# Performance work log

Hardware: AMD Instinct MI355X
Metric: run time of the kernel (lower is better)

## Reference

```python
import jax, jax.numpy as jnp
import numpy as np

N_EMBD = 1024
N_HEAD = 16
HEAD_SIZE = N_EMBD // N_HEAD
B, T = 2, 2048
LN_EPS = 1e-5


def _layernorm(x, g, b):
    mu = jnp.mean(x, axis=-1, keepdims=True)
    var = jnp.var(x, axis=-1, keepdims=True)
    return (x - mu) * jax.lax.rsqrt(var + LN_EPS) * g + b


def setup_inputs() -> dict:
    key = jax.random.key(0)
    ks = jax.random.split(key, 12)
    s_in = 1.0 / np.sqrt(N_EMBD)
    s_ff = 1.0 / np.sqrt(4 * N_EMBD)
    return {
        "x": jax.random.normal(ks[0], (B, T, N_EMBD), jnp.float32),
        # per-head q/k/v linears stacked head-major: [n_embd, n_embd]
        "Wq": jax.random.uniform(ks[1], (N_EMBD, N_EMBD), jnp.float32, -s_in, s_in),
        "Wk": jax.random.uniform(ks[2], (N_EMBD, N_EMBD), jnp.float32, -s_in, s_in),
        "Wv": jax.random.uniform(ks[3], (N_EMBD, N_EMBD), jnp.float32, -s_in, s_in),
        "Wo": jax.random.uniform(ks[4], (N_EMBD, N_EMBD), jnp.float32, -s_in, s_in),
        "bo": jax.random.uniform(ks[5], (N_EMBD,), jnp.float32, -s_in, s_in),
        "W1": jax.random.uniform(ks[6], (N_EMBD, 4 * N_EMBD), jnp.float32, -s_in, s_in),
        "b1": jax.random.uniform(ks[7], (4 * N_EMBD,), jnp.float32, -s_in, s_in),
        "W2": jax.random.uniform(ks[8], (4 * N_EMBD, N_EMBD), jnp.float32, -s_ff, s_ff),
        "b2": jax.random.uniform(ks[9], (N_EMBD,), jnp.float32, -s_ff, s_ff),
        "g1": jnp.ones((N_EMBD,), jnp.float32),
        "be1": jnp.zeros((N_EMBD,), jnp.float32),
        "g2": jnp.ones((N_EMBD,), jnp.float32),
        "be2": jnp.zeros((N_EMBD,), jnp.float32),
    }


def reference(x, Wq, Wk, Wv, Wo, bo, W1, b1, W2, b2, g1, be1, g2, be2):
    Bx, Tx, C = x.shape
    # --- self-attention on ln1(x) ---
    h = _layernorm(x, g1, be1)
    q = (h @ Wq).reshape(Bx, Tx, N_HEAD, HEAD_SIZE)
    k = (h @ Wk).reshape(Bx, Tx, N_HEAD, HEAD_SIZE)
    v = (h @ Wv).reshape(Bx, Tx, N_HEAD, HEAD_SIZE)
    # NOTE: faithful to source -- scale uses full C (n_embd), not head_size
    scale = C ** (-0.5)
    wei = jnp.einsum("bqhd,bkhd->bhqk", q, k) * scale  # [B,H,T,T]
    causal = jnp.tril(jnp.ones((Tx, Tx), bool))
    wei = jnp.where(causal, wei, -jnp.inf)
    wei = jax.nn.softmax(wei, axis=-1)
    attn = jnp.einsum("bhqk,bkhd->bqhd", wei, v).reshape(Bx, Tx, C)
    x = x + (attn @ Wo + bo)
    # --- feed-forward on ln2(x) ---
    h2 = _layernorm(x, g2, be2)
    x = x + (jax.nn.relu(h2 @ W1 + b1) @ W2 + b2)
    return x
```

## Files before the change

### kernel.cpp

```cpp
#include <hip/hip_runtime.h>
#include <hip/hip_bf16.h>
#include <math.h>

#define BB 2
#define TT 2048
#define CC 1024
#define NH 16
#define HD 64
#define BT (BB*TT)
#define LN_EPS 1e-5f
#define ATT_SCALE 0.03125f

typedef __bf16 bf16x8 __attribute__((ext_vector_type(8)));
typedef __bf16 bf16x4 __attribute__((ext_vector_type(4)));
typedef short shortx4 __attribute__((ext_vector_type(4)));
typedef float floatx4 __attribute__((ext_vector_type(4)));

__device__ __forceinline__ void gl_lds16(const __bf16* g, __bf16* l) {
    __builtin_amdgcn_global_load_lds((const __attribute__((address_space(1))) void*)g,
                                     (__attribute__((address_space(3))) void*)l,
                                     16, 0, 0);
}

#define MFMA32(a, b, c) __builtin_amdgcn_mfma_f32_16x16x32_bf16(a, b, c, 0, 0, 0)

#if __has_builtin(__builtin_amdgcn_mfma_f32_16x16x16_bf16)
__device__ __forceinline__ floatx4 mfma16(bf16x4 a, bf16x4 b, floatx4 c) {
    return __builtin_amdgcn_mfma_f32_16x16x16_bf16(a, b, c, 0, 0, 0);
}
#else
__device__ __forceinline__ floatx4 mfma16(bf16x4 a, bf16x4 b, floatx4 c) {
    return __builtin_amdgcn_mfma_f32_16x16x16bf16_1k(
        __builtin_bit_cast(shortx4, a), __builtin_bit_cast(shortx4, b), c, 0, 0, 0);
}
#endif

#define BARRIER() __builtin_amdgcn_s_barrier()
#define MEMF()  asm volatile("" ::: "memory")
#define LGKM0() asm volatile("s_waitcnt lgkmcnt(0)" ::: "memory")
#define VM4()   asm volatile("s_waitcnt vmcnt(4)" ::: "memory")
#define VM0()   asm volatile("s_waitcnt vmcnt(0)" ::: "memory")

__device__ __forceinline__ void swizzle_xcd(int& xb, int& yb, int& zb) {
    int nx = gridDim.x, ny = gridDim.y;
    int total = nx * ny * (int)gridDim.z;
    int lin = blockIdx.x + nx * (blockIdx.y + ny * blockIdx.z);
    int c = lin & 7, s = lin >> 3;
    int idx = c * (total >> 3) + s;
    xb = idx % nx;
    yb = (idx / nx) % ny;
    zb = idx / (nx * ny);
}

__global__ __launch_bounds__(256) void transpose_ln(
        const float* __restrict__ Wq, const float* __restrict__ Wk,
        const float* __restrict__ Wv, const float* __restrict__ Wo,
        const float* __restrict__ W1, const float* __restrict__ W2,
        __bf16* __restrict__ WqkvT, __bf16* __restrict__ WoT,
        __bf16* __restrict__ W1T, __bf16* __restrict__ W2T,
        const float* __restrict__ x, const float* __restrict__ g1,
        const float* __restrict__ be1, __bf16* __restrict__ hb) {
    __shared__ float t[32][33];
    __shared__ float rs_[4], rss_[4];
    __shared__ float mu_s, inv_s;
    int idx = blockIdx.x;
    if (idx >= 12288) {
        int row = idx - 12288;
        const float4* xr = (const float4*)(x + (size_t)row * CC);
        float4 v = xr[threadIdx.x];
        float s  = v.x + v.y + v.z + v.w;
        float ss = v.x*v.x + v.y*v.y + v.z*v.z + v.w*v.w;
        #pragma unroll
        for (int off = 32; off; off >>= 1) {
            s  += __shfl_down(s, off);
            ss += __shfl_down(ss, off);
        }
        int lane = threadIdx.x & 63, wid = threadIdx.x >> 6;
        if (lane == 0) { rs_[wid] = s; rss_[wid] = ss; }
        __syncthreads();
        if (threadIdx.x == 0) {
            float S  = rs_[0] + rs_[1] + rs_[2] + rs_[3];
            float SS = rss_[0] + rss_[1] + rss_[2] + rss_[3];
            float mu  = S * (1.0f / CC);
            float var = SS * (1.0f / CC) - mu * mu;
            mu_s  = mu;
            inv_s = rsqrtf(var + LN_EPS);
        }
        __syncthreads();
        float mu = mu_s, inv = inv_s;
        float4 gv = ((const float4*)g1)[threadIdx.x];
        float4 bv = ((const float4*)be1)[threadIdx.x];
        bf16x4 o;
        o[0] = (__bf16)((v.x - mu) * inv * gv.x + bv.x);
        o[1] = (__bf16)((v.y - mu) * inv * gv.y + bv.y);
        o[2] = (__bf16)((v.z - mu) * inv * gv.z + bv.z);
        o[3] = (__bf16)((v.w - mu) * inv * gv.w + bv.w);
        *(bf16x4*)(hb + (size_t)row * CC + threadIdx.x * 4) = o;
        return;
    }
    const float* src; __bf16* dst; int K, N, tn, tk;
    if (idx < 3072) {
        int wsel = idx >> 10, local = idx & 1023;
        src = (wsel == 0) ? Wq : (wsel == 1 ? Wk : Wv);
        dst = WqkvT + (size_t)wsel * 1024 * 1024;
        K = 1024; N = 1024; tn = local & 31; tk = local >> 5;
    } else if (idx < 4096) {
        int local = idx - 3072;
        src = Wo; dst = WoT; K = 1024; N = 1024; tn = local & 31; tk = local >> 5;
    } else if (idx < 8192) {
        int local = idx - 4096;
        src = W1; dst = W1T; K = 1024; N = 4096; tn = local & 127; tk = local >> 7;
    } else {
        int local = idx - 8192;
        src = W2; dst = W2T; K = 4096; N = 1024; tn = local & 31; tk = local >> 5;
    }
    int n0 = tn * 32, k0 = tk * 32;
    int tx = threadIdx.x & 31, ty = threadIdx.x >> 5;
    #pragma unroll
    for (int r = ty; r < 32; r += 8)
        t[r][tx] = src[(size_t)(k0 + r) * N + n0 + tx];
    __syncthreads();
    #pragma unroll
    for (int r = ty; r < 32; r += 8)
        dst[(size_t)(n0 + r) * K + k0 + tx] = (__bf16)t[tx][r];
}

__global__ __launch_bounds__(256) void reduce_wo_ln(const __bf16* __restrict__ P,
                                                    const float* __restrict__ bo,
                                                    const float* __restrict__ x,
                                                    const float* __restrict__ g2,
                                                    const float* __restrict__ be2,
                                                    float* __restrict__ x2,
                                                    __bf16* __restrict__ hb) {
    int row = blockIdx.x;
    int c = threadIdx.x * 4;
    const size_t S = (size_t)BT * CC;
    float4 xb = *(const float4*)(x + (size_t)row * CC + c);
    float4 bb = *(const float4*)(bo + c);
    float4 v;
    v.x = xb.x + bb.x;
    v.y = xb.y + bb.y;
    v.z = xb.z + bb.z;
    v.w = xb.w + bb.w;
    #pragma unroll
    for (int z = 0; z < 4; ++z) {
        bf16x4 a = *(const bf16x4*)(P + z * S + (size_t)row * CC + c);
        v.x += (float)a[0]; v.y += (float)a[1]; v.z += (float)a[2]; v.w += (float)a[3];
    }
    *(float4*)(x2 + (size_t)row * CC + c) = v;

    float s  = v.x + v.y + v.z + v.w;
    float ss = v.x*v.x + v.y*v.y + v.z*v.z + v.w*v.w;
    #pragma unroll
    for (int off = 32; off; off >>= 1) {
        s  += __shfl_down(s, off);
        ss += __shfl_down(ss, off);
    }
    __shared__ float rs_[4], rss_[4];
    __shared__ float mu_s, inv_s;
    int lane = threadIdx.x & 63, wid = threadIdx.x >> 6;
    if (lane == 0) { rs_[wid] = s; rss_[wid] = ss; }
    __syncthreads();
    if (threadIdx.x == 0) {
        float S_  = rs_[0] + rs_[1] + rs_[2] + rs_[3];
        float SS = rss_[0] + rss_[1] + rss_[2] + rss_[3];
        float mu  = S_ * (1.0f / CC);
        float var = SS * (1.0f / CC) - mu * mu;
        mu_s  = mu;
        inv_s = rsqrtf(var + LN_EPS);
    }
    __syncthreads();
    float mu = mu_s, inv = inv_s;
    float4 gv = ((const float4*)g2)[threadIdx.x];
    float4 bv = ((const float4*)be2)[threadIdx.x];
    bf16x4 o;
    o[0] = (__bf16)((v.x - mu) * inv * gv.x + bv.x);
    o[1] = (__bf16)((v.y - mu) * inv * gv.y + bv.y);
    o[2] = (__bf16)((v.z - mu) * inv * gv.z + bv.z);
    o[3] = (__bf16)((v.w - mu) * inv * gv.w + bv.w);
    *(bf16x4*)(hb + (size_t)row * CC + c) = o;
}

__global__ __launch_bounds__(256) void reduce_ffn(const __bf16* __restrict__ P,
                                                  const float* __restrict__ b2,
                                                  const float* __restrict__ x2,
                                                  float* __restrict__ out) {
    int row = blockIdx.x;
    int c = threadIdx.x * 4;
    const size_t S = (size_t)BT * CC;
    float4 v = *(const float4*)(x2 + (size_t)row * CC + c);
    float4 bb = *(const float4*)(b2 + c);
    v.x += bb.x; v.y += bb.y; v.z += bb.z; v.w += bb.w;
    #pragma unroll
    for (int z = 0; z < 4; ++z) {
        bf16x4 a = *(const bf16x4*)(P + z * S + (size_t)row * CC + c);
        v.x += (float)a[0]; v.y += (float)a[1]; v.z += (float)a[2]; v.w += (float)a[3];
    }
    *(float4*)(out + (size_t)row * CC + c) = v;
}

__device__ __forceinline__ void stage_half(const __bf16* __restrict__ mat, int row0,
                                           int ldk, int k0, __bf16* lds, int tid) {
    int r = tid >> 3;
    int lch = (tid & 7) ^ (r & 7);
    const __bf16* gp = mat + (size_t)(row0 + r) * ldk + k0 + lch * 8;
    gl_lds16(gp, lds + tid * 8);
    gl_lds16(gp + (size_t)64 * ldk, lds + 4096 + tid * 8);
}

__device__ __forceinline__ void load_a(const __bf16* As_, int qr, int wr, int m, int g,
                                       bf16x8 (&fa)[4][2]) {
    #pragma unroll
    for (int i = 0; i < 4; ++i) {
        int ra = qr * 128 + wr * 64 + i * 16 + m;
        #pragma unroll
        for (int kk = 0; kk < 2; ++kk)
            fa[i][kk] = *(const bf16x8*)&As_[ra * 64 + (((kk * 4 + g) ^ (m & 7)) * 8)];
    }
}

__device__ __forceinline__ void load_b(const __bf16* Bs_, int qc, int wc, int m, int g,
                                       bf16x8 (&fb)[2][2]) {
    #pragma unroll
    for (int j = 0; j < 2; ++j) {
        int rb = qc * 128 + wc * 32 + j * 16 + m;
        #pragma unroll
        for (int kk = 0; kk < 2; ++kk)
            fb[j][kk] = *(const bf16x8*)&Bs_[rb * 64 + (((kk * 4 + g) ^ (m & 7)) * 8)];
    }
}

__device__ __forceinline__ void mfma_q(bf16x8 (&fa)[4][2], bf16x8 (&fb)[2][2],
                                       floatx4 (&a)[4][2]) {
    __builtin_amdgcn_s_setprio(1);
    #pragma unroll
    for (int i = 0; i < 4; ++i)
        #pragma unroll
        for (int j = 0; j < 2; ++j)
            #pragma unroll
            for (int kk = 0; kk < 2; ++kk)
                a[i][j] = MFMA32(fa[i][kk], fb[j][kk], a[i][j]);
    __builtin_amdgcn_s_setprio(0);
}

template<int SK, typename OT, bool BIAS, bool RELU, bool VSPLIT>
__global__ __launch_bounds__(512, 2) void gemm256(const __bf16* __restrict__ A,
                                                  const __bf16* __restrict__ Bt,
                                                  const float* __restrict__ bias,
                                                  OT* __restrict__ C,
                                                  __bf16* __restrict__ vt,
                                                  int M, int N, int K) {
    __shared__ __bf16 As[2][16384];
    __shared__ __bf16 Bs[2][16384];
    int bx, by, bz;
    swizzle_xcd(bx, by, bz);
    const int tid = threadIdx.x;
    const int l = tid & 63, w = tid >> 6;
    const int m = l & 15, g = l >> 4;
    const int wr = w >> 2, wc = w & 3;
    const int m0 = by * 256, n0 = bx * 256;
    const int Keff = K / SK;
    const int kb = (SK > 1) ? bz * Keff : 0;
    const int iters = Keff >> 7;

    floatx4 acc[2][2][4][2];
    #pragma unroll
    for (int a = 0; a < 2; ++a)
        #pragma unroll
        for (int b = 0; b < 2; ++b)
            #pragma unroll
            for (int i = 0; i < 4; ++i)
                #pragma unroll
                for (int j = 0; j < 2; ++j) {
                    floatx4 z = {0.f, 0.f, 0.f, 0.f};
                    acc[a][b][i][j] = z;
                }

    stage_half(A,  m0,       K, kb,      &As[0][0],    tid);
    stage_half(Bt, n0,       K, kb,      &Bs[0][0],    tid);
    stage_half(Bt, n0 + 128, K, kb,      &Bs[0][8192], tid);
    stage_half(A,  m0 + 128, K, kb,      &As[0][8192], tid);
    stage_half(A,  m0,       K, kb + 64, &As[1][0],    tid);
    stage_half(Bt, n0 + 128, K, kb + 64, &Bs[1][8192], tid);
    VM4(); BARRIER(); MEMF();

    bf16x8 fa[4][2], fbA[2][2], fbB[2][2];

    for (int it = 0; it < iters; ++it) {
        const bool lastI = (it == iters - 1);
        const int kB = kb + (2 * it + 1) * 64;
        const int kC = kB + 64;
        const int kD = kC + 64;

        load_a(&As[0][0], 0, wr, m, g, fa);
        load_b(&Bs[0][0], 0, wc, m, g, fbA);
        stage_half(Bt, n0, K, kB, &Bs[1][0], tid);
        BARRIER(); LGKM0(); mfma_q(fa, fbA, acc[0][0]); BARRIER(); MEMF();
        load_b(&Bs[0][0], 1, wc, m, g, fbB);
        stage_half(A, m0 + 128, K, kB, &As[1][8192], tid);
        BARRIER(); LGKM0(); mfma_q(fa, fbB, acc[0][1]); BARRIER(); MEMF();
        load_a(&As[0][0], 1, wr, m, g, fa);
        if (!lastI) stage_half(A, m0, K, kC, &As[0][0], tid);
        BARRIER(); LGKM0(); mfma_q(fa, fbB, acc[1][1]); BARRIER(); MEMF();
        if (!lastI) { stage_half(Bt, n0 + 128, K, kC, &Bs[0][8192], tid);
                      VM4(); }
        else VM0();
        BARRIER(); mfma_q(fa, fbA, acc[1][0]); BARRIER(); MEMF();

        load_a(&As[1][0], 0, wr, m, g, fa);
        load_b(&Bs[1][0], 0, wc, m, g, fbA);
        if (!lastI) stage_half(Bt, n0, K, kC, &Bs[0][0], tid);
        BARRIER(); LGKM0(); mfma_q(fa, fbA, acc[0][0]); BARRIER(); MEMF();
        load_b(&Bs[1][0], 1, wc, m, g, fbB);
        if (!lastI) stage_half(A, m0 + 128, K, kC, &As[0][8192], tid);
        BARRIER(); LGKM0(); mfma_q(fa, fbB, acc[0][1]); BARRIER(); MEMF();
        load_a(&As[1][0], 1, wr, m, g, fa);
        if (!lastI) stage_half(A, m0, K, kD, &As[1][0], tid);
        BARRIER(); LGKM0(); mfma_q(fa, fbB, acc[1][1]); BARRIER(); MEMF();
        if (!lastI) { stage_half(Bt, n0 + 128, K, kD, &Bs[1][8192], tid);
                      VM4(); }
        BARRIER(); mfma_q(fa, fbA, acc[1][0]); BARRIER(); MEMF();
    }

    if (SK > 1) {
        __bf16* P = (__bf16*)C + (size_t)bz * M * N;
        #pragma unroll
        for (int qr = 0; qr < 2; ++qr)
            #pragma unroll
            for (int i = 0; i < 4; ++i) {
                int row = m0 + qr * 128 + wr * 64 + i * 16 + g * 4;
                #pragma unroll
                for (int qc = 0; qc < 2; ++qc)
                    #pragma unroll
                    for (int j = 0; j < 2; ++j) {
                        int col = n0 + qc * 128 + wc * 32 + j * 16 + m;
                        #pragma unroll
                        for (int r = 0; r < 4; ++r)
                            P[(size_t)(row + r) * N + col] = (__bf16)acc[qr][qc][i][j][r];
                    }
            }
    } else if (VSPLIT && n0 >= 2048) {
        #pragma unroll
        for (int qr = 0; qr < 2; ++qr)
            #pragma unroll
            for (int i = 0; i < 4; ++i) {
                int row = m0 + qr * 128 + wr * 64 + i * 16 + g * 4;
                int bb = row >> 11, t0 = row & 2047;
                #pragma unroll
                for (int qc = 0; qc < 2; ++qc)
                    #pragma unroll
                    for (int j = 0; j < 2; ++j) {
                        int cv = n0 + qc * 128 + wc * 32 + j * 16 + m - 2048;
                        bf16x4 o;
                        #pragma unroll
                        for (int r = 0; r < 4; ++r) o[r] = (__bf16)acc[qr][qc][i][j][r];
                        *(bf16x4*)(vt + ((size_t)(bb * NH + (cv >> 6)) * HD + (cv & 63)) * 2048 + t0) = o;
                    }
            }
    } else {
        #pragma unroll
        for (int qr = 0; qr < 2; ++qr)
            #pragma unroll
            for (int i = 0; i < 4; ++i) {
                int row = m0 + qr * 128 + wr * 64 + i * 16 + g * 4;
                #pragma unroll
                for (int qc = 0; qc < 2; ++qc)
                    #pragma unroll
                    for (int j = 0; j < 2; ++j) {
                        int col = n0 + qc * 128 + wc * 32 + j * 16 + m;
                        float bv = BIAS ? bias[col] : 0.0f;
                        #pragma unroll
                        for (int r = 0; r < 4; ++r) {
                            float vo = acc[qr][qc][i][j][r] + bv;
                            if (RELU) vo = fmaxf(vo, 0.0f);
                            if (VSPLIT && col < 1024) vo *= ATT_SCALE;
                            C[(size_t)(row + r) * N + col] = (OT)vo;
                        }
                    }
            }
    }
}

__global__ __launch_bounds__(256, 4) void attn_mfma5(const __bf16* __restrict__ qkv,
                                                     const __bf16* __restrict__ vt,
                                                     __bf16* __restrict__ att) {
    const int lin = blockIdx.x;
    const int q0 = lin & 15, h = (lin >> 4) & 15, b = (lin >> 8) & 1, half = lin >> 9;
    const int qs = half ? 31 - q0 : q0;

    const int tid = threadIdx.x;
    const int l = tid & 63, w = tid >> 6;
    const int m = l & 15, g = l >> 4;

    __shared__ __bf16 Ks[2][128][32];
    __shared__ __bf16 Vt3[8][64][16];

    const __bf16* qp = qkv + (size_t)b * TT * 3072 + h * HD;
    const __bf16* kp = qp + 1024;
    const __bf16* vh = vt + (size_t)(b * NH + h) * HD * 2048;

    bf16x8 qb0, qb1;
    {
        int qrow = qs * 64 + w * 16 + m;
        qb0 = *(const bf16x8*)(qp + (size_t)qrow * 3072 + g * 8);
        qb1 = *(const bf16x8*)(qp + (size_t)qrow * 3072 + 32 + g * 8);
    }

    floatx4 O[4];
    float l_s = 0.0f;
    #pragma unroll
    for (int jd = 0; jd < 4; ++jd) { floatx4 z = {0.f, 0.f, 0.f, 0.f}; O[jd] = z; }

    const int ktmax = qs >> 1;
    for (int kt = 0; kt <= ktmax; ++kt) {
        __syncthreads();
        #pragma unroll
        for (int c = 0; c < 4; ++c) {
            int idx = w * 4 + c;
            int dh = idx >> 3, k16 = idx & 7;
            gl_lds16(kp + (size_t)(kt * 128 + k16 * 16 + (l >> 2)) * 3072
                        + dh * 32 + (((l & 3) ^ ((l >> 3) & 3)) * 8),
                     (__bf16*)Ks + dh * 4096 + k16 * 512);
        }
        #pragma unroll
        for (int c = 0; c < 4; ++c) {
            int idx = w * 4 + c;
            int jt = idx >> 1, dhf = idx & 1;
            gl_lds16(vh + (size_t)(dhf * 32 + (l >> 1)) * 2048 + kt * 128
                        + jt * 16 + (((l & 1) ^ ((l >> 3) & 1)) * 8),
                     (__bf16*)Vt3 + jt * 1024 + dhf * 512);
        }
        __syncthreads();

        floatx4 S[8];
        #pragma unroll
        for (int jt = 0; jt < 8; ++jt) {
            int co = (g ^ ((m >> 1) & 3)) * 8;
            bf16x8 kf0 = *(const bf16x8*)&Ks[0][jt * 16 + m][co];
            bf16x8 kf1 = *(const bf16x8*)&Ks[1][jt * 16 + m][co];
            floatx4 z = {0.f, 0.f, 0.f, 0.f};
            z = MFMA32(kf0, qb0, z);
            S[jt] = MFMA32(kf1, qb1, z);
        }

        const bool last = (kt == ktmax);
        if (last) {
            int qr = (qs & 1) * 64 + w * 16 + m;
            #pragma unroll
            for (int jt = 0; jt < 8; ++jt)
                #pragma unroll
                for (int r = 0; r < 4; ++r)
                    if (jt * 16 + g * 4 + r > qr) S[jt][r] = -1e30f;
        }
        bf16x4 pv[8];
        #pragma unroll
        for (int jt = 0; jt < 8; ++jt) {
            bf16x4 t;
            #pragma unroll
            for (int r = 0; r < 4; ++r) {
                float p = __expf(S[jt][r]);
                l_s += p;
                t[r] = (__bf16)p;
            }
            pv[jt] = t;
        }

        #pragma unroll
        for (int jt = 0; jt < 8; ++jt)
            #pragma unroll
            for (int jd = 0; jd < 4; ++jd) {
                bf16x4 vf = *(const bf16x4*)&Vt3[jt][jd * 16 + m]
                                [((g >> 1) ^ ((m >> 2) & 1)) * 8 + (g & 1) * 4];
                O[jd] = mfma16(vf, pv[jt], O[jd]);
            }
    }

    float lsum = l_s;
    lsum += __shfl_xor(lsum, 16, 64);
    lsum += __shfl_xor(lsum, 32, 64);
    float inv = 1.0f / lsum;
    int qrow = qs * 64 + w * 16 + m;
    #pragma unroll
    for (int jd = 0; jd < 4; ++jd) {
        bf16x4 o;
        #pragma unroll
        for (int r = 0; r < 4; ++r) o[r] = (__bf16)(O[jd][r] * inv);
        *(bf16x4*)(att + ((size_t)b * TT + qrow) * CC + h * HD + jd * 16 + g * 4) = o;
    }
}

extern "C" void kernel_launch(void* const* d_in, const int* in_sizes, int n_in,
                              void* d_out, int out_size, void* d_ws, size_t ws_size,
                              hipStream_t stream) {
    const float* x   = (const float*)d_in[0];
    const float* Wq  = (const float*)d_in[1];
    const float* Wk  = (const float*)d_in[2];
    const float* Wv  = (const float*)d_in[3];
    const float* Wo  = (const float*)d_in[4];
    const float* bo  = (const float*)d_in[5];
    const float* W1  = (const float*)d_in[6];
    const float* b1  = (const float*)d_in[7];
    const float* W2  = (const float*)d_in[8];
    const float* b2  = (const float*)d_in[9];
    const float* g1  = (const float*)d_in[10];
    const float* be1 = (const float*)d_in[11];
    const float* g2  = (const float*)d_in[12];
    const float* be2 = (const float*)d_in[13];
    float* out = (float*)d_out;

    char* p = (char*)d_ws;
    char*   pool  = p;          p += (size_t)32 * 1024 * 1024;
    __bf16* qkvb  = (__bf16*)pool;
    __bf16* vtb   = (__bf16*)(pool + (size_t)BT * 3072 * 2);
    __bf16* wop   = (__bf16*)pool;
    __bf16* ffp   = (__bf16*)pool;
    __bf16* attb  = (__bf16*)p; p += (size_t)BT * CC * 2;
    __bf16* hb    = (__bf16*)p; p += (size_t)BT * CC * 2;
    float*  x2    = (float*)p;  p += (size_t)BT * CC * 4;
    __bf16* ffb   = (__bf16*)p; p += (size_t)BT * 4096 * 2;
    __bf16* WqkvT = (__bf16*)p; p += (size_t)3072 * 1024 * 2;
    __bf16* WoT   = (__bf16*)p; p += (size_t)1024 * 1024 * 2;
    __bf16* W1T   = (__bf16*)p; p += (size_t)4096 * 1024 * 2;
    __bf16* W2T   = (__bf16*)p; p += (size_t)1024 * 4096 * 2;

    transpose_ln<<<16384, 256, 0, stream>>>(Wq, Wk, Wv, Wo, W1, W2,
                                            WqkvT, WoT, W1T, W2T,
                                            x, g1, be1, hb);
    gemm256<1, __bf16, false, false, true><<<dim3(12, 16), 512, 0, stream>>>(
        hb, WqkvT, nullptr, qkvb, vtb, BT, 3072, 1024);
    attn_mfma5<<<1024, 256, 0, stream>>>(qkvb, vtb, attb);
    gemm256<4, __bf16, false, false, false><<<dim3(4, 16, 4), 512, 0, stream>>>(
        attb, WoT, nullptr, wop, nullptr, BT, 1024, 1024);
    reduce_wo_ln<<<BT, 256, 0, stream>>>(wop, bo, x, g2, be2, x2, hb);
    gemm256<1, __bf16, true, true, false><<<dim3(16, 16), 512, 0, stream>>>(
        hb, W1T, b1, ffb, nullptr, BT, 4096, 1024);
    gemm256<4, __bf16, false, false, false><<<dim3(4, 16, 4), 512, 0, stream>>>(
        ffb, W2T, nullptr, ffp, nullptr, BT, 1024, 4096);
    reduce_ffn<<<BT, 256, 0, stream>>>(ffp, b2, x2, out);
}
```

Before: 321.8 us.

## Prefetch V tiles into registers and remap attention block-to-head ordering

Result: slower. 329.4 us (+2.4%).

```diff
diff --git a/kernel.cpp b/kernel.cpp
--- a/kernel.cpp
+++ b/kernel.cpp
@@ -381,11 +381,14 @@
     }
 }
 
-__global__ __launch_bounds__(256, 4) void attn_mfma5(const __bf16* __restrict__ qkv,
+__global__ __launch_bounds__(256, 4) void attn_mfma6(const __bf16* __restrict__ qkv,
                                                      const __bf16* __restrict__ vt,
                                                      __bf16* __restrict__ att) {
-    const int lin = blockIdx.x;
-    const int q0 = lin & 15, h = (lin >> 4) & 15, b = (lin >> 8) & 1, half = lin >> 9;
+    const int p = blockIdx.x;
+    const int h    = (p & 7) + 8 * ((p >> 7) & 1);
+    const int q0   = (p >> 3) & 15;
+    const int b    = (p >> 8) & 1;
+    const int half = p >> 9;
     const int qs = half ? 31 - q0 : q0;
 
     const int tid = threadIdx.x;
@@ -398,6 +401,11 @@
     const __bf16* qp = qkv + (size_t)b * TT * 3072 + h * HD;
     const __bf16* kp = qp + 1024;
     const __bf16* vh = vt + (size_t)(b * NH + h) * HD * 2048;
+
+    const int jts = tid >> 5;
+    const int r5  = tid & 31;
+    const int d0  = r5 * 2;
+    const __bf16* vbase = vh + (size_t)d0 * 2048 + jts * 16;
 
     bf16x8 qb0, qb1;
     {
@@ -410,6 +418,12 @@
     float l_s = 0.0f;
     #pragma unroll
     for (int jd = 0; jd < 4; ++jd) { floatx4 z = {0.f, 0.f, 0.f, 0.f}; O[jd] = z; }
+
+    bf16x8 vreg[4];
+    vreg[0] = *(const bf16x8*)(vbase);
+    vreg[1] = *(const bf16x8*)(vbase + 8);
+    vreg[2] = *(const bf16x8*)(vbase + 2048);
+    vreg[3] = *(const bf16x8*)(vbase + 2048 + 8);
 
     const int ktmax = qs >> 1;
     for (int kt = 0; kt <= ktmax; ++kt) {
@@ -423,14 +437,27 @@
                      (__bf16*)Ks + dh * 4096 + k16 * 512);
         }
         #pragma unroll
-        for (int c = 0; c < 4; ++c) {
-            int idx = w * 4 + c;
-            int jt = idx >> 1, dhf = idx & 1;
-            gl_lds16(vh + (size_t)(dhf * 32 + (l >> 1)) * 2048 + kt * 128
-                        + jt * 16 + (((l & 1) ^ ((l >> 3) & 1)) * 8),
-                     (__bf16*)Vt3 + jt * 1024 + dhf * 512);
+        for (int dd = 0; dd < 2; ++dd) {
+            int d = d0 + dd;
+            int s16 = (d >> 2) & 1, s8 = (d >> 3) & 1;
+            #pragma unroll
+            for (int sl = 0; sl < 2; ++sl) {
+                bf16x8 v = vreg[dd * 2 + sl];
+                if (s8) {
+                    bf16x8 t = {v[4], v[5], v[6], v[7], v[0], v[1], v[2], v[3]};
+                    v = t;
+                }
+                *(bf16x8*)&Vt3[jts][d][(sl ^ s16) * 8] = v;
+            }
         }
         __syncthreads();
+        if (kt < ktmax) {
+            const __bf16* vs = vbase + (kt + 1) * 128;
+            vreg[0] = *(const bf16x8*)(vs);
+            vreg[1] = *(const bf16x8*)(vs + 8);
+            vreg[2] = *(const bf16x8*)(vs + 2048);
+            vreg[3] = *(const bf16x8*)(vs + 2048 + 8);
+        }
 
         floatx4 S[8];
         #pragma unroll
@@ -458,9 +485,9 @@
             bf16x4 t;
             #pragma unroll
             for (int r = 0; r < 4; ++r) {
-                float p = __expf(S[jt][r]);
-                l_s += p;
-                t[r] = (__bf16)p;
+                float p2 = __expf(S[jt][r]);
+                l_s += p2;
+                t[r] = (__bf16)p2;
             }
             pv[jt] = t;
         }
@@ -470,7 +497,7 @@
             #pragma unroll
             for (int jd = 0; jd < 4; ++jd) {
                 bf16x4 vf = *(const bf16x4*)&Vt3[jt][jd * 16 + m]
-                                [((g >> 1) ^ ((m >> 2) & 1)) * 8 + (g & 1) * 4];
+                        [((g >> 1) ^ ((m >> 2) & 1)) * 8 + ((g & 1) ^ ((m >> 3) & 1)) * 4];
                 O[jd] = mfma16(vf, pv[jt], O[jd]);
             }
     }
@@ -528,7 +555,7 @@
                                             x, g1, be1, hb);
     gemm256<1, __bf16, false, false, true><<<dim3(12, 16), 512, 0, stream>>>(
         hb, WqkvT, nullptr, qkvb, vtb, BT, 3072, 1024);
-    attn_mfma5<<<1024, 256, 0, stream>>>(qkvb, vtb, attb);
+    attn_mfma6<<<1024, 256, 0, stream>>>(qkvb, vtb, attb);
     gemm256<4, __bf16, false, false, false><<<dim3(4, 16, 4), 512, 0, stream>>>(
         attb, WoT, nullptr, wop, nullptr, BT, 1024, 1024);
     reduce_wo_ln<<<BT, 256, 0, stream>>>(wop, bo, x, g2, be2, x2, hb);
```
